# Kernel optimization log

Hardware: AMD Instinct MI355X
Metric: run time of the kernel (lower is better)

## Reference

```python
import math
import jax, jax.numpy as jnp
import numpy as np

EPS = 1e-4
FMAX = 18  # max filtersize for scale clamped to 2.5: ceil(3*2^2.5+0.5)=18 -> kernel 37x37
KSZ = 2 * FMAX + 1


def _conv2d(x, w, b):
    # 3x3 conv, padding 1, NCHW / OIHW (cross-correlation, matches torch)
    y = jax.lax.conv_general_dilated(x, w, (1, 1), [(1, 1), (1, 1)],
                                     dimension_numbers=('NCHW', 'OIHW', 'NCHW'))
    return y + b[None, :, None, None]


def _basis_filters(scale):
    # scale: [B] -> [B,3,K,K] (g, dgdx, dgdy), masked to the per-sample support
    std = 2.0 ** scale                              # [B]
    fs = jnp.ceil(3.0 * std + 0.5)                  # per-sample filtersize
    x = jnp.arange(-FMAX, FMAX + 1, dtype=jnp.float32)          # [K]
    m = (jnp.abs(x)[None, :] <= fs[:, None]).astype(jnp.float32)  # [B,K] support mask
    e = jnp.exp(-0.5 * (x[None, :] / std[:, None]) ** 2) * m      # masked 1D gaussian [B,K]
    g = e[:, :, None] * e[:, None, :]                              # [B,K,K]
    g = g / jnp.sum(g, axis=(1, 2), keepdims=True)
    c = (-x[None, :] / (std[:, None] ** 3 * 2.0 * math.pi)) * e    # [B,K]
    dgdx = c[:, :, None] * e[:, None, :]   # varies along first spatial dim (x[0])
    dgdx = dgdx / jnp.sum(jnp.abs(dgdx), axis=(1, 2), keepdims=True)
    dgdy = e[:, :, None] * c[:, None, :]   # varies along second spatial dim (x[1])
    dgdy = dgdy / jnp.sum(jnp.abs(dgdy), axis=(1, 2), keepdims=True)
    return jnp.stack([g, dgdx, dgdy], axis=1)  # [B,3,K,K]


def setup_inputs() -> dict:
    key = jax.random.key(0)
    ks = jax.random.split(key, 7)
    B, H, W = 8, 512, 512
    batch = jax.random.uniform(ks[0], (B, 3, H, W), dtype=jnp.float32)
    gcm = jnp.array([[0.06, 0.63, 0.27], [0.3, 0.04, -0.35], [0.34, -0.6, 0.17]],
                    dtype=jnp.float32)
    w1 = jax.random.normal(ks[1], (16, 3, 3, 3), dtype=jnp.float32) * 0.1
    b1 = jax.random.normal(ks[2], (16,), dtype=jnp.float32) * 0.01
    w2 = jax.random.normal(ks[3], (16, 16, 3, 3), dtype=jnp.float32) * 0.1
    b2 = jax.random.normal(ks[4], (16,), dtype=jnp.float32) * 0.01
    w3 = jax.random.normal(ks[5], (1, 16, 3, 3), dtype=jnp.float32) * 0.1
    b3 = jax.random.normal(ks[6], (1,), dtype=jnp.float32) * 0.01
    return {"batch": batch, "gcm": gcm, "w1": w1, "b1": b1,
            "w2": w2, "b2": b2, "w3": w3, "b3": b3}


def reference(batch, gcm, w1, b1, w2, b2, w3, b3):
    B, _, H, W = batch.shape
    # ---- RGB order prior (non-differentiable, no_grad in torch) ----
    oh = lambda i: jax.nn.one_hot(i, 3, axis=1, dtype=batch.dtype)
    mx = jnp.argmax(batch, axis=1)                 # first max
    mn = jnp.argmin(batch, axis=1)
    bf = batch[:, ::-1]
    mx2 = 2 - jnp.argmax(bf, axis=1)               # last max
    mn2 = 2 - jnp.argmin(bf, axis=1)
    RGB_order = jax.lax.stop_gradient(
        0.5 * (oh(mx) + oh(mx2)) - 0.5 * (oh(mn) + oh(mn2)))  # [B,3,H,W]

    # ---- per-sample adaptive scale from small CNN ----
    h = jax.nn.silu(_conv2d(batch, w1, b1))
    h = jax.nn.silu(_conv2d(h, w2, b2))
    s = _conv2d(h, w3, b3)
    scale = jnp.clip(jnp.mean(s, axis=(1, 2, 3)), -2.5, 2.5)   # [B]

    # ---- Gaussian color model ----
    xg = jnp.einsum('ij,bjhw->bihw', gcm, batch)  # [B,3,H,W] -> (E, El, Ell)

    # ---- per-sample Gaussian basis convolution, batched via grouped conv ----
    basis = _basis_filters(scale)                                  # [B,3,K,K]
    xin = xg.reshape(1, B * 3, H, W)
    wk = jnp.broadcast_to(basis[:, None], (B, 3, 3, KSZ, KSZ)).reshape(B * 9, 1, KSZ, KSZ)
    out = jax.lax.conv_general_dilated(xin, wk, (1, 1), [(FMAX, FMAX), (FMAX, FMAX)],
                                       feature_group_count=B * 3,
                                       dimension_numbers=('NCHW', 'OIHW', 'NCHW'))
    out = out.reshape(B, 3, 3, H, W)   # [B, chan(E/El/Ell), filt(g/dx/dy), H, W]
    E = out[:, 0, 0:1]
    Ex = out[:, 0, 1:2]
    Ey = out[:, 0, 2:3]
    El = out[:, 1, 0:1]
    Ell = out[:, 2, 0:1]

    Hf = jnp.arctan(El / (Ell + EPS))
    S = jnp.log((El ** 2 + Ell ** 2) / (E ** 2 + EPS) + EPS)
    Ww = jnp.arctan((Ex / (E + EPS)) ** 2 + (Ey / (E + EPS)) ** 2)
    return jnp.concatenate([Hf, S, RGB_order, Ww], axis=1)  # [B,6,H,W]
```

## Files before the change

kernel.cpp:

```cpp
#include <hip/hip_runtime.h>
#include <hip/hip_bf16.h>

constexpr int BN = 8, HH = 512, WW = 512;
constexpr int PIX = HH * WW;
constexpr float EPSF = 1e-4f;

__device__ __forceinline__ float b2f(__hip_bfloat16 x) { return __bfloat162float(x); }
__device__ __forceinline__ __hip_bfloat16 f2b(float x) { return __float2bfloat16(x); }
__device__ __forceinline__ unsigned short bfbits(float x) {
    union { __hip_bfloat16 b; unsigned short u; } cv; cv.b = f2b(x); return cv.u;
}
__device__ __forceinline__ unsigned int cvtpk(float lo, float hi) {
    unsigned int r;
    asm("v_cvt_pk_bf16_f32 %0, %1, %2" : "=v"(r) : "v"(lo), "v"(hi));
    return r;
}
__device__ __forceinline__ float silu(float a) {
    return a * __builtin_amdgcn_rcpf(1.f + __expf(-a));
}

typedef __attribute__((ext_vector_type(8))) short bf16x8;
typedef __attribute__((ext_vector_type(4))) float f32x4;

constexpr int OFF_TOT = 0;
constexpr int OFF_ROW0 = 128;
constexpr int OFF_ROW1 = 256;
constexpr int OFF_COL0 = 384;
constexpr int OFF_COL1 = 512;
constexpr int OFF_COR = 640;
constexpr int OFF_W1R = 1280;
constexpr int OFF_WR  = 2048;
constexpr int OFF_EH  = 4608;
constexpr int OFF_CH  = 5120;
constexpr size_t OFF_TPB = 65536;
constexpr size_t TP_BYTES = (size_t)4 * BN * PIX * 4;
constexpr size_t WS_NEEDED = OFF_TPB + TP_BYTES;

__global__ void prep_kernel(const float* __restrict__ w1, const float* __restrict__ w2,
                            float* __restrict__ wsf) {
    int t = threadIdx.x;
    for (int i = t; i < 640; i += 256) wsf[i] = 0.f;
    unsigned short* ab = (unsigned short*)(wsf + OFF_WR);
    for (int idx = t; idx < 5120; idx += 256) {
        int part = idx / 2560;
        int id = idx - part * 2560;
        int ks = id >> 9, rem = id & 511, lane = rem >> 3, j = id & 7;
        int oc = lane & 15, q = lane >> 4;
        int k = q * 8 + j;
        int tap = 2 * ks + (k >> 4), ic = k & 15;
        float val = (tap <= 8) ? w2[oc * 144 + ic * 9 + tap] : 0.f;
        float hv = b2f(f2b(val));
        ab[idx] = (part == 0) ? bfbits(val) : bfbits(val - hv);
    }
    unsigned short* a1 = (unsigned short*)(wsf + OFF_W1R);
    for (int idx = t; idx < 1024; idx += 256) {
        int part = idx >> 9;
        int id = idx & 511;
        int lane = id >> 3, j = id & 7;
        int oc = lane & 15, q = lane >> 4;
        int k = q * 8 + j;
        float val = (k < 27) ? w1[oc * 27 + k] : 0.f;
        float hv = b2f(f2b(val));
        a1[idx] = (part == 0) ? bfbits(val) : bfbits(val - hv);
    }
}

__global__ __launch_bounds__(256) void conv12_kernel(const float* __restrict__ batch,
                                                     const unsigned short* __restrict__ w1buf,
                                                     const float* __restrict__ b1,
                                                     const unsigned short* __restrict__ abuf,
                                                     const float* __restrict__ b2v,
                                                     float* __restrict__ wsf,
                                                     float* __restrict__ out) {
    __shared__ unsigned short stb[3][12][68];
    __shared__ uint4 h1s[10 * 66 * 2];
    __shared__ float part[4][16];

    int tx = threadIdx.x;
    int lane = tx & 63, wave = tx >> 6;
    int n = lane & 15, q = lane >> 4;
    int w0 = blockIdx.x * 64, h0 = blockIdx.y * 8, b = blockIdx.z;

    union { uint4 u; bf16x8 v; } cv;
    const float* pb = batch + (size_t)(b * 3) * PIX;

    unsigned int* stw = (unsigned int*)&stb[0][0][0];
    for (int i = tx; i < 1224; i += 256) {
        int ch = i / 408, rem = i - ch * 408;
        int r = rem / 34, c2 = rem - r * 34;
        int gh = h0 - 2 + r, gw = w0 - 2 + 2 * c2;
        const float* p = pb + (size_t)ch * PIX + (size_t)gh * WW;
        bool rok = (gh >= 0) && (gh < HH);
        float v0 = (rok && gw >= 0 && gw < WW) ? p[gw] : 0.f;
        float v1 = (rok && gw + 1 >= 0 && gw + 1 < WW) ? p[gw + 1] : 0.f;
        stw[i] = cvtpk(v0, v1);
    }

    bf16x8 w1h, w1l;
    const uint4* w14 = (const uint4*)w1buf;
    cv.u = w14[lane];      w1h = cv.v;
    cv.u = w14[64 + lane]; w1l = cv.v;
    int koff[8];
#pragma unroll
    for (int j = 0; j < 8; j++) {
        int k = q * 8 + j;
        int kk = (k < 27) ? k : 0;
        int ic = kk / 9, rem = kk - ic * 9, kh = rem / 3, kw = rem - kh * 3;
        koff[j] = ic * 816 + kh * 68 + kw;
    }
    float b1q[4];
#pragma unroll
    for (int r = 0; r < 4; r++) b1q[r] = b1[q * 4 + r];
    bool hiq = (q == 3);
    __syncthreads();

    const unsigned short* sptr = &stb[0][0][0];
    unsigned int* hw = (unsigned int*)h1s;
    int i_c = wave * 16 + n;
    int r_c = (unsigned)i_c / 66u; int c_c = i_c - r_c * 66;
    int base_c = r_c * 68 + c_c;
    unsigned short x0 = sptr[base_c + koff[0]], x1 = sptr[base_c + koff[1]];
    unsigned short x2 = sptr[base_c + koff[2]], x3 = sptr[base_c + koff[3]];
    unsigned short x4 = sptr[base_c + koff[4]], x5 = sptr[base_c + koff[5]];
    unsigned short x6 = sptr[base_c + koff[6]], x7 = sptr[base_c + koff[7]];
    int g = wave;
    for (int gi = 0; gi < 11; gi++) {
        unsigned short y0 = 0, y1 = 0, y2 = 0, y3 = 0, y4 = 0, y5 = 0, y6 = 0, y7 = 0;
        int i_n = 0, c_n = 0;
        if (gi < 10) {
            i_n = (g + 4) * 16 + n; if (i_n > 659) i_n = 659;
            int r_n = (unsigned)i_n / 66u; c_n = i_n - r_n * 66;
            int base_n = r_n * 68 + c_n;
            y0 = sptr[base_n + koff[0]]; y1 = sptr[base_n + koff[1]];
            y2 = sptr[base_n + koff[2]]; y3 = sptr[base_n + koff[3]];
            y4 = sptr[base_n + koff[4]]; y5 = sptr[base_n + koff[5]];
            y6 = sptr[base_n + koff[6]]; y7 = sptr[base_n + koff[7]];
        }
        union { unsigned int w[4]; bf16x8 v; } bb;
        bb.w[0] = (unsigned int)x0 | ((unsigned int)x1 << 16);
        bb.w[1] = (unsigned int)x2 | ((unsigned int)x3 << 16);
        bb.w[2] = (unsigned int)x4 | ((unsigned int)x5 << 16);
        bb.w[3] = (unsigned int)x6 | ((unsigned int)x7 << 16);
        if (hiq) {
            bb.w[1] &= 0xFFFFu; bb.w[2] = 0u; bb.w[3] = 0u;
        }
        f32x4 a = {0, 0, 0, 0};
        a = __builtin_amdgcn_mfma_f32_16x16x32_bf16(w1h, bb.v, a, 0, 0, 0);
        a = __builtin_amdgcn_mfma_f32_16x16x32_bf16(w1l, bb.v, a, 0, 0, 0);
        int rr_ = (unsigned)i_c / 66u;
        int gh = h0 - 1 + rr_, gw = w0 - 1 + c_c;
        bool ok = ((unsigned)gh < (unsigned)HH) && ((unsigned)gw < (unsigned)WW);
        unsigned int p0 = cvtpk(silu(a[0] + b1q[0]), silu(a[1] + b1q[1]));
        unsigned int p1 = cvtpk(silu(a[2] + b1q[2]), silu(a[3] + b1q[3]));
        p0 = ok ? p0 : 0u;
        p1 = ok ? p1 : 0u;
        int swz = (c_c >> 2) & 1;
        int slot = i_c * 2 + ((q >= 2) ? (swz ^ 1) : swz);
        *(uint2*)&hw[slot * 4 + (q & 1) * 2] = make_uint2(p0, p1);
        x0 = y0; x1 = y1; x2 = y2; x3 = y3; x4 = y4; x5 = y5; x6 = y6; x7 = y7;
        i_c = i_n; c_c = c_n;
        g += 4;
    }

    for (int j = tx; j < 512; j += 256) {
        int rr = j >> 6, ccx = j & 63;
        size_t p = (size_t)(h0 + rr) * WW + (w0 + ccx);
        float v0 = pb[p], v1 = pb[(size_t)PIX + p], v2 = pb[2 * (size_t)PIX + p];
        int mx  = (v0 >= v1 && v0 >= v2) ? 0 : ((v1 >= v2) ? 1 : 2);
        int mx2 = (v2 >= v1 && v2 >= v0) ? 2 : ((v1 >= v0) ? 1 : 0);
        int mn  = (v0 <= v1 && v0 <= v2) ? 0 : ((v1 <= v2) ? 1 : 2);
        int mn2 = (v2 <= v1 && v2 <= v0) ? 2 : ((v1 <= v0) ? 1 : 0);
#pragma unroll
        for (int c = 0; c < 3; c++) {
            float r = 0.5f * ((float)(c == mx) + (float)(c == mx2))
                    - 0.5f * ((float)(c == mn) + (float)(c == mn2));
            out[(size_t)(b * 6 + 2 + c) * PIX + p] = r;
        }
    }
    __syncthreads();

    bf16x8 ah[5], al[5];
    const uint4* ab4 = (const uint4*)abuf;
#pragma unroll
    for (int ks = 0; ks < 5; ks++) {
        cv.u = ab4[ks * 64 + lane];       ah[ks] = cv.v;
        cv.u = ab4[320 + ks * 64 + lane]; al[ks] = cv.v;
    }
    float b2q[4];
#pragma unroll
    for (int r = 0; r < 4; r++) b2q[r] = b2v[q * 4 + r];

    float tt[4] = {0, 0, 0, 0};
    float cs0[4] = {0, 0, 0, 0};
    float cs1[4] = {0, 0, 0, 0};
    for (int rloc = 0; rloc < 2; rloc++) {
        int row = wave * 2 + rloc;
        int grow = h0 + row;
        f32x4 acc[4] = {{0,0,0,0},{0,0,0,0},{0,0,0,0},{0,0,0,0}};
#pragma unroll
        for (int ks = 0; ks < 5; ks++) {
            int tap = 2 * ks + (q >> 1); if (tap > 8) tap = 8;
            int dh = tap / 3 - 1, dw = tap % 3 - 1;
            int half = q & 1;
            int lr = row + 1 + dh;
#pragma unroll
            for (int t = 0; t < 4; t++) {
                int c = 1 + dw + t * 16 + n;
                cv.u = h1s[(lr * 66 + c) * 2 + (half ^ ((c >> 2) & 1))];
                acc[t] = __builtin_amdgcn_mfma_f32_16x16x32_bf16(ah[ks], cv.v, acc[t], 0, 0, 0);
                acc[t] = __builtin_amdgcn_mfma_f32_16x16x32_bf16(al[ks], cv.v, acc[t], 0, 0, 0);
            }
        }
        float sv[4][4];
#pragma unroll
        for (int t = 0; t < 4; t++)
#pragma unroll
            for (int r = 0; r < 4; r++)
                sv[t][r] = silu(acc[t][r] + b2q[r]);
#pragma unroll
        for (int r = 0; r < 4; r++) tt[r] += sv[0][r] + sv[1][r] + sv[2][r] + sv[3][r];
        if (grow == 0 || grow == HH - 1) {
            int off = (grow == 0) ? OFF_ROW0 : OFF_ROW1;
#pragma unroll
            for (int r = 0; r < 4; r++) {
                float x = sv[0][r] + sv[1][r] + sv[2][r] + sv[3][r];
#pragma unroll
                for (int d = 1; d < 16; d <<= 1) x += __shfl_xor(x, d, 64);
                if (n == 0) atomicAdd(&wsf[off + b * 16 + q * 4 + r], x);
            }
        }
        if (blockIdx.x == 0 && n == 0)
#pragma unroll
            for (int r = 0; r < 4; r++) cs0[r] += sv[0][r];
        if (blockIdx.x == 7 && n == 15)
#pragma unroll
            for (int r = 0; r < 4; r++) cs1[r] += sv[3][r];
        if ((grow == 0 || grow == HH - 1)) {
            int hi = (grow == 0) ? 0 : 1;
            if (blockIdx.x == 0 && n == 0)
#pragma unroll
                for (int r = 0; r < 4; r++)
                    wsf[OFF_COR + ((b * 2 + hi) * 2 + 0) * 16 + q * 4 + r] = sv[0][r];
            if (blockIdx.x == 7 && n == 15)
#pragma unroll
                for (int r = 0; r < 4; r++)
                    wsf[OFF_COR + ((b * 2 + hi) * 2 + 1) * 16 + q * 4 + r] = sv[3][r];
        }
    }
    if (blockIdx.x == 0 && n == 0)
#pragma unroll
        for (int r = 0; r < 4; r++) atomicAdd(&wsf[OFF_COL0 + b * 16 + q * 4 + r], cs0[r]);
    if (blockIdx.x == 7 && n == 15)
#pragma unroll
        for (int r = 0; r < 4; r++) atomicAdd(&wsf[OFF_COL1 + b * 16 + q * 4 + r], cs1[r]);
#pragma unroll
    for (int r = 0; r < 4; r++) {
        float x = tt[r];
#pragma unroll
        for (int d = 1; d < 16; d <<= 1) x += __shfl_xor(x, d, 64);
        tt[r] = x;
    }
    if (n == 0)
#pragma unroll
        for (int r = 0; r < 4; r++) part[wave][q * 4 + r] = tt[r];
    __syncthreads();
    if (tx < 16)
        atomicAdd(&wsf[OFF_TOT + b * 16 + tx],
                  part[0][tx] + part[1][tx] + part[2][tx] + part[3][tx]);
}

__global__ void filter_kernel(const float* __restrict__ w3, const float* __restrict__ b3,
                              float* __restrict__ wsf) {
    int b = blockIdx.x, t = threadIdx.x;
    __shared__ float red[160];
    float val = 0.f;
    if (t < 144) {
        int ic = t / 9, tap = t % 9, kh = tap / 3, kw = tap % 3;
        float T = wsf[OFF_TOT + b * 16 + ic];
        int hi = -1, wi = -1;
        if (kh == 0) { T -= wsf[OFF_ROW1 + b * 16 + ic]; hi = 1; }
        else if (kh == 2) { T -= wsf[OFF_ROW0 + b * 16 + ic]; hi = 0; }
        if (kw == 0) { T -= wsf[OFF_COL1 + b * 16 + ic]; wi = 1; }
        else if (kw == 2) { T -= wsf[OFF_COL0 + b * 16 + ic]; wi = 0; }
        if (hi >= 0 && wi >= 0) T += wsf[OFF_COR + ((b * 2 + hi) * 2 + wi) * 16 + ic];
        val = w3[t] * T;
    }
    red[t] = val;
    __syncthreads();
    __shared__ float sh_mean;
    if (t == 0) {
        float S = 0.f;
        for (int i = 0; i < 144; i++) S += red[i];
        sh_mean = b3[0] + S * (1.f / (float)PIX);
    }
    __syncthreads();
    float scale = fminf(2.5f, fmaxf(-2.5f, sh_mean));
    float sd = exp2f(scale);
    float fs = ceilf(3.f * sd + 0.5f);
    float e = 0.f, c = 0.f;
    if (t < 37) {
        float x = (float)(t - 18);
        if (fabsf(x) <= fs) {
            float qq = x / sd;
            e = __expf(-0.5f * qq * qq);
            c = -x / (sd * sd * sd * 6.28318530717958647692f) * e;
        }
    }
    __shared__ float sa[40], sb[40];
    if (t < 37) { sa[t] = e; sb[t] = fabsf(c); }
    __syncthreads();
    __shared__ float Se, Sc;
    if (t == 0) {
        float a = 0.f, d = 0.f;
        for (int i = 0; i < 37; i++) { a += sa[i]; d += sb[i]; }
        Se = a; Sc = d;
    }
    __syncthreads();
    if (t < 37) {
        wsf[OFF_EH + b * 37 + t] = e / Se;
        wsf[OFF_CH + b * 37 + t] = c / Sc;
    }
}

__device__ __forceinline__ int skw(int c) { return c + (c >> 5); }
__global__ __launch_bounds__(256, 4) void horiz_kernel(const float* __restrict__ batch,
                                                       const float* __restrict__ gcm,
                                                       const float* __restrict__ ehat,
                                                       const float* __restrict__ chat,
                                                       float* __restrict__ t) {
    __shared__ float xr[2][3][566];
    __shared__ float cE[40], cC[40];
    int tx = threadIdx.x;
    int h0 = blockIdx.x * 2;
    int b  = blockIdx.y;
    if (tx < 37) { cE[tx] = ehat[b * 37 + tx]; cC[tx] = chat[b * 37 + tx]; }
    const float* pb = batch + (size_t)(b * 3) * PIX;
    float g0 = gcm[0], g1 = gcm[1], g2 = gcm[2];
    float g3 = gcm[3], g4 = gcm[4], g5 = gcm[5];
    float g6 = gcm[6], g7 = gcm[7], g8 = gcm[8];
    for (int i = tx; i < 2 * 548; i += 256) {
        int r = i / 548, c = i - r * 548;
        int gw = c - 18;
        float v0 = 0.f, v1 = 0.f, v2 = 0.f;
        if (gw >= 0 && gw < WW) {
            size_t p = (size_t)(h0 + r) * WW + gw;
            v0 = pb[p]; v1 = pb[(size_t)PIX + p]; v2 = pb[2 * (size_t)PIX + p];
        }
        int cs = skw(c);
        xr[r][0][cs] = g0 * v0 + g1 * v1 + g2 * v2;
        xr[r][1][cs] = g3 * v0 + g4 * v1 + g5 * v2;
        xr[r][2][cs] = g6 * v0 + g7 * v1 + g8 * v2;
    }
    __syncthreads();
    int r = tx >> 7, colbase = (tx & 127) * 4;
    float a0[4] = {}, a1[4] = {}, a2[4] = {}, a3[4] = {};
    float e1, e2, e3, d1, d2, d3;
    {
        float ce[3], cc2[3];
#pragma unroll
        for (int k = 0; k < 3; k++) { ce[k] = cE[k]; cc2[k] = cC[k]; }
#pragma unroll
        for (int kk = 0; kk < 3; kk++) {
            int cs = skw(colbase + kk);
            float x0 = xr[r][0][cs], x1 = xr[r][1][cs], x2 = xr[r][2][cs];
#pragma unroll
            for (int i = 0; i < 3; i++) {
                if (i <= kk) {
                    float ce_ = ce[kk - i], cc_ = cc2[kk - i];
                    a0[i] += ce_ * x0; a1[i] += ce_ * x1;
                    a2[i] += ce_ * x2; a3[i] += cc_ * x0;
                }
            }
        }
        e1 = ce[2]; e2 = ce[1]; e3 = ce[0];
        d1 = cc2[2]; d2 = cc2[1]; d3 = cc2[0];
    }
#pragma unroll 2
    for (int kk = 3; kk < 37; kk++) {
        float e0 = cE[kk], d0 = cC[kk];
        int cs = skw(colbase + kk);
        float x0 = xr[r][0][cs], x1 = xr[r][1][cs], x2 = xr[r][2][cs];
        a0[0] += e0 * x0; a1[0] += e0 * x1; a2[0] += e0 * x2; a3[0] += d0 * x0;
        a0[1] += e1 * x0; a1[1] += e1 * x1; a2[1] += e1 * x2; a3[1] += d1 * x0;
        a0[2] += e2 * x0; a1[2] += e2 * x1; a2[2] += e2 * x2; a3[2] += d2 * x0;
        a0[3] += e3 * x0; a1[3] += e3 * x1; a2[3] += e3 * x2; a3[3] += d3 * x0;
        e3 = e2; e2 = e1; e1 = e0; d3 = d2; d2 = d1; d1 = d0;
    }
    {
        int cs = skw(colbase + 37);
        float x0 = xr[r][0][cs], x1 = xr[r][1][cs], x2 = xr[r][2][cs];
        a0[1] += e1 * x0; a1[1] += e1 * x1; a2[1] += e1 * x2; a3[1] += d1 * x0;
        a0[2] += e2 * x0; a1[2] += e2 * x1; a2[2] += e2 * x2; a3[2] += d2 * x0;
        a0[3] += e3 * x0; a1[3] += e3 * x1; a2[3] += e3 * x2; a3[3] += d3 * x0;
    }
    {
        int cs = skw(colbase + 38);
        float x0 = xr[r][0][cs], x1 = xr[r][1][cs], x2 = xr[r][2][cs];
        a0[2] += e1 * x0; a1[2] += e1 * x1; a2[2] += e1 * x2; a3[2] += d1 * x0;
        a0[3] += e2 * x0; a1[3] += e2 * x1; a2[3] += e2 * x2; a3[3] += d2 * x0;
    }
    {
        int cs = skw(colbase + 39);
        float x0 = xr[r][0][cs], x1 = xr[r][1][cs], x2 = xr[r][2][cs];
        a0[3] += e1 * x0; a1[3] += e1 * x1; a2[3] += e1 * x2; a3[3] += d1 * x0;
    }
    const size_t PL = (size_t)BN * PIX;
    size_t p = (size_t)b * PIX + (size_t)(h0 + r) * WW + colbase;
    *(float4*)&t[0 * PL + p] = make_float4(a0[0], a0[1], a0[2], a0[3]);
    *(float4*)&t[1 * PL + p] = make_float4(a1[0], a1[1], a1[2], a1[3]);
    *(float4*)&t[2 * PL + p] = make_float4(a2[0], a2[1], a2[2], a2[3]);
    *(float4*)&t[3 * PL + p] = make_float4(a3[0], a3[1], a3[2], a3[3]);
}

#define VACC(ee, dd, ii) { E[ii] += (ee) * v0; Ex[ii] += (dd) * v0; Ey[ii] += (ee) * v3; \
                           El[ii] += (ee) * v1; Ell[ii] += (ee) * v2; }
__global__ __launch_bounds__(256, 4) void vert_kernel(const float* __restrict__ t,
                                                      const float* __restrict__ ehat,
                                                      const float* __restrict__ chat,
                                                      float* __restrict__ out) {
    __shared__ float cE[40], cC[40];
    int tx = threadIdx.x;
    int b = blockIdx.z;
    if (tx < 37) { cE[tx] = ehat[b * 37 + tx]; cC[tx] = chat[b * 37 + tx]; }
    int j = blockIdx.x * 64 + (tx & 63);
    int r0 = (blockIdx.y * 4 + (tx >> 6)) * 4;
    const size_t PL = (size_t)BN * PIX;
    const float* t0 = t + (size_t)b * PIX;
    __syncthreads();
    float E[4] = {}, Ex[4] = {}, Ey[4] = {}, El[4] = {}, Ell[4] = {};
    bool safe = (r0 >= 18) && (r0 <= HH - 22);
    float e1, e2, e3, d1, d2, d3;
    {
        float ce[3], cc2[3];
#pragma unroll
        for (int k = 0; k < 3; k++) { ce[k] = cE[k]; cc2[k] = cC[k]; }
#pragma unroll
        for (int kk = 0; kk < 3; kk++) {
            int gr = r0 - 18 + kk;
            float v0 = 0.f, v1 = 0.f, v2 = 0.f, v3 = 0.f;
            if ((unsigned)gr < (unsigned)HH) {
                size_t idx = (size_t)gr * WW + j;
                v0 = t0[idx]; v1 = t0[PL + idx]; v2 = t0[2 * PL + idx]; v3 = t0[3 * PL + idx];
            }
#pragma unroll
            for (int i = 0; i < 3; i++) {
                if (i <= kk) {
                    float ee = ce[kk - i], dd = cc2[kk - i];
                    VACC(ee, dd, i)
                }
            }
        }
        e1 = ce[2]; e2 = ce[1]; e3 = ce[0];
        d1 = cc2[2]; d2 = cc2[1]; d3 = cc2[0];
    }
    const float* pv = t0 + (size_t)(r0 - 15) * WW + j;
    if (safe) {
#pragma unroll 2
        for (int kk = 3; kk < 37; kk++) {
            float e0 = cE[kk], d0 = cC[kk];
            float v0 = pv[0], v1 = pv[PL], v2 = pv[2 * PL], v3 = pv[3 * PL];
            VACC(e0, d0, 0) VACC(e1, d1, 1) VACC(e2, d2, 2) VACC(e3, d3, 3)
            e3 = e2; e2 = e1; e1 = e0; d3 = d2; d2 = d1; d1 = d0;
            pv += WW;
        }
    } else {
        int gr = r0 - 15;
#pragma unroll 2
        for (int kk = 3; kk < 37; kk++) {
            float e0 = cE[kk], d0 = cC[kk];
            float v0 = 0.f, v1 = 0.f, v2 = 0.f, v3 = 0.f;
            if ((unsigned)gr < (unsigned)HH) {
                v0 = pv[0]; v1 = pv[PL]; v2 = pv[2 * PL]; v3 = pv[3 * PL];
            }
            VACC(e0, d0, 0) VACC(e1, d1, 1) VACC(e2, d2, 2) VACC(e3, d3, 3)
            e3 = e2; e2 = e1; e1 = e0; d3 = d2; d2 = d1; d1 = d0;
            pv += WW; gr++;
        }
    }
#pragma unroll
    for (int kk = 37; kk < 40; kk++) {
        int gr = r0 - 18 + kk;
        float v0 = 0.f, v1 = 0.f, v2 = 0.f, v3 = 0.f;
        if (gr < HH) {
            size_t idx = (size_t)gr * WW + j;
            v0 = t0[idx]; v1 = t0[PL + idx]; v2 = t0[2 * PL + idx]; v3 = t0[3 * PL + idx];
        }
        if (kk == 37) { VACC(e1, d1, 1) VACC(e2, d2, 2) VACC(e3, d3, 3) }
        if (kk == 38) { VACC(e1, d1, 2) VACC(e2, d2, 3) }
        if (kk == 39) { VACC(e1, d1, 3) }
    }
#pragma unroll
    for (int i = 0; i < 4; i++) {
        int h = r0 + i;
        float Hf = atanf(El[i] / (Ell[i] + EPSF));
        float S = logf((El[i] * El[i] + Ell[i] * Ell[i]) / (E[i] * E[i] + EPSF) + EPSF);
        float rx = Ex[i] / (E[i] + EPSF), ry = Ey[i] / (E[i] + EPSF);
        float Wv = atanf(rx * rx + ry * ry);
        size_t base = (size_t)(b * 6) * PIX + (size_t)h * WW + j;
        out[base] = Hf;
        out[base + PIX] = S;
        out[base + 5 * (size_t)PIX] = Wv;
    }
}
#undef VACC

extern "C" void kernel_launch(void* const* d_in, const int* in_sizes, int n_in,
                              void* d_out, int out_size, void* d_ws, size_t ws_size,
                              hipStream_t stream) {
    const float* batch = (const float*)d_in[0];
    const float* gcm   = (const float*)d_in[1];
    const float* w1    = (const float*)d_in[2];
    const float* b1    = (const float*)d_in[3];
    const float* w2    = (const float*)d_in[4];
    const float* b2    = (const float*)d_in[5];
    const float* w3    = (const float*)d_in[6];
    const float* b3    = (const float*)d_in[7];
    float* out = (float*)d_out;

    if (ws_size < WS_NEEDED) return;

    float* wsf = (float*)d_ws;
    float* tpl = (float*)((char*)d_ws + OFF_TPB);
    float* ehat = wsf + OFF_EH;
    float* chat = wsf + OFF_CH;

    prep_kernel<<<dim3(1), dim3(256), 0, stream>>>(w1, w2, wsf);
    conv12_kernel<<<dim3(8, 64, 8), dim3(256), 0, stream>>>(
        batch, (const unsigned short*)(wsf + OFF_W1R), b1,
        (const unsigned short*)(wsf + OFF_WR), b2, wsf, out);
    filter_kernel<<<dim3(8), dim3(160), 0, stream>>>(w3, b3, wsf);
    horiz_kernel<<<dim3(256, 8), dim3(256), 0, stream>>>(batch, gcm, ehat, chat, tpl);
    vert_kernel<<<dim3(8, 32, 8), dim3(256), 0, stream>>>(tpl, ehat, chat, out);
}
```

Before: 233.0 us.

## Run separable Gaussian convolutions as banded bf16 MFMA matmuls with split precision

The horizontal and vertical 37-tap passes move from scalar FMA loops onto MFMA. The filter kernel now builds banded Toeplitz A-fragments of the 1D Gaussian and its derivative, split into bf16 hi/mid/lo parts. Inputs are split into bf16 components so the products approach fp32 accuracy. The intermediate is stored transposed, with bf16 for the E and Ey planes and fp32 for El/Ell. This replaces many FMAs with fewer matrix instructions and cuts intermediate traffic, at the cost of lower precision on some planes and extra splitting work.

```diff
diff --git a/kernel.cpp b/kernel.cpp
--- a/kernel.cpp
+++ b/kernel.cpp
@@ -10,6 +10,9 @@
 __device__ __forceinline__ unsigned short bfbits(float x) {
     union { __hip_bfloat16 b; unsigned short u; } cv; cv.b = f2b(x); return cv.u;
 }
+__device__ __forceinline__ float ubf(unsigned short u) {
+    union { unsigned int i; float f; } c; c.i = ((unsigned int)u) << 16; return c.f;
+}
 __device__ __forceinline__ unsigned int cvtpk(float lo, float hi) {
     unsigned int r;
     asm("v_cvt_pk_bf16_f32 %0, %1, %2" : "=v"(r) : "v"(lo), "v"(hi));
@@ -21,6 +24,16 @@
 
 typedef __attribute__((ext_vector_type(8))) short bf16x8;
 typedef __attribute__((ext_vector_type(4))) float f32x4;
+
+#define MF(acc, A, B) (acc) = __builtin_amdgcn_mfma_f32_16x16x32_bf16((A), (B), (acc), 0, 0, 0)
+
+__device__ __forceinline__ bf16x8 ldb(const unsigned short* s, int off16) {
+    const uint2* p = (const uint2*)(s + off16);
+    uint2 a = p[0], c = p[1];
+    union { uint4 u; bf16x8 v; } cv;
+    cv.u = make_uint4(a.x, a.y, c.x, c.y);
+    return cv.v;
+}
 
 constexpr int OFF_TOT = 0;
 constexpr int OFF_ROW0 = 128;
@@ -30,11 +43,14 @@
 constexpr int OFF_COR = 640;
 constexpr int OFF_W1R = 1280;
 constexpr int OFF_WR  = 2048;
-constexpr int OFF_EH  = 4608;
-constexpr int OFF_CH  = 5120;
-constexpr size_t OFF_TPB = 65536;
-constexpr size_t TP_BYTES = (size_t)4 * BN * PIX * 4;
-constexpr size_t WS_NEEDED = OFF_TPB + TP_BYTES;
+constexpr int OFF_AFR = 8192;
+constexpr size_t OFF_TP0 = 262144;
+constexpr size_t SZ_TPH = (size_t)BN * PIX * 2;
+constexpr size_t SZ_TPF = (size_t)BN * PIX * 4;
+constexpr size_t OFF_TP1 = OFF_TP0 + SZ_TPH;
+constexpr size_t OFF_TP2 = OFF_TP1 + SZ_TPF;
+constexpr size_t OFF_TP3 = OFF_TP2 + SZ_TPF;
+constexpr size_t WS_NEEDED = OFF_TP3 + SZ_TPH;
 
 __global__ void prep_kernel(const float* __restrict__ w1, const float* __restrict__ w2,
                             float* __restrict__ wsf) {
@@ -145,8 +161,8 @@
             bb.w[1] &= 0xFFFFu; bb.w[2] = 0u; bb.w[3] = 0u;
         }
         f32x4 a = {0, 0, 0, 0};
-        a = __builtin_amdgcn_mfma_f32_16x16x32_bf16(w1h, bb.v, a, 0, 0, 0);
-        a = __builtin_amdgcn_mfma_f32_16x16x32_bf16(w1l, bb.v, a, 0, 0, 0);
+        MF(a, w1h, bb.v);
+        MF(a, w1l, bb.v);
         int rr_ = (unsigned)i_c / 66u;
         int gh = h0 - 1 + rr_, gw = w0 - 1 + c_c;
         bool ok = ((unsigned)gh < (unsigned)HH) && ((unsigned)gw < (unsigned)WW);
@@ -207,8 +223,8 @@
             for (int t = 0; t < 4; t++) {
                 int c = 1 + dw + t * 16 + n;
                 cv.u = h1s[(lr * 66 + c) * 2 + (half ^ ((c >> 2) & 1))];
-                acc[t] = __builtin_amdgcn_mfma_f32_16x16x32_bf16(ah[ks], cv.v, acc[t], 0, 0, 0);
-                acc[t] = __builtin_amdgcn_mfma_f32_16x16x32_bf16(al[ks], cv.v, acc[t], 0, 0, 0);
+                MF(acc[t], ah[ks], cv.v);
+                MF(acc[t], al[ks], cv.v);
             }
         }
         float sv[4][4];
@@ -306,203 +322,197 @@
             c = -x / (sd * sd * sd * 6.28318530717958647692f) * e;
         }
     }
-    __shared__ float sa[40], sb[40];
-    if (t < 37) { sa[t] = e; sb[t] = fabsf(c); }
+    __shared__ float sa[40], sb2[40];
+    if (t < 37) { sa[t] = e; sb2[t] = fabsf(c); }
     __syncthreads();
     __shared__ float Se, Sc;
     if (t == 0) {
         float a = 0.f, d = 0.f;
-        for (int i = 0; i < 37; i++) { a += sa[i]; d += sb[i]; }
+        for (int i = 0; i < 37; i++) { a += sa[i]; d += sb2[i]; }
         Se = a; Sc = d;
     }
     __syncthreads();
-    if (t < 37) {
-        wsf[OFF_EH + b * 37 + t] = e / Se;
-        wsf[OFF_CH + b * 37 + t] = c / Sc;
-    }
-}
-
-__device__ __forceinline__ int skw(int c) { return c + (c >> 5); }
-__global__ __launch_bounds__(256, 4) void horiz_kernel(const float* __restrict__ batch,
-                                                       const float* __restrict__ gcm,
-                                                       const float* __restrict__ ehat,
-                                                       const float* __restrict__ chat,
-                                                       float* __restrict__ t) {
-    __shared__ float xr[2][3][566];
-    __shared__ float cE[40], cC[40];
+    __shared__ float sEn[37], sCn[37];
+    if (t < 37) { sEn[t] = e / Se; sCn[t] = c / Sc; }
+    __syncthreads();
+    if (t < 64) {
+        int r = t & 15, q = t >> 4;
+        uint4* afr = (uint4*)(wsf + OFF_AFR) + (size_t)b * 640 + t;
+#pragma unroll
+        for (int ks = 0; ks < 2; ks++) {
+            unsigned short eh[8], em[8], el[8], chp[8], cmp[8];
+#pragma unroll
+            for (int j2 = 0; j2 < 8; j2++) {
+                int d = ks * 32 + q * 8 + j2 - r;
+                bool ok = (d >= 0) && (d <= 36);
+                float ve = ok ? sEn[ok ? d : 0] : 0.f;
+                float vc = ok ? sCn[ok ? d : 0] : 0.f;
+                eh[j2] = bfbits(ve);
+                float r1 = ve - ubf(eh[j2]);
+                em[j2] = bfbits(r1);
+                el[j2] = bfbits(r1 - ubf(em[j2]));
+                chp[j2] = bfbits(vc);
+                cmp[j2] = bfbits(vc - ubf(chp[j2]));
+            }
+#define PK2(a0, a1) ((unsigned)(a0) | ((unsigned)(a1) << 16))
+            afr[(ks * 3 + 0) * 64] = make_uint4(PK2(eh[0], eh[1]), PK2(eh[2], eh[3]), PK2(eh[4], eh[5]), PK2(eh[6], eh[7]));
+            afr[(ks * 3 + 1) * 64] = make_uint4(PK2(em[0], em[1]), PK2(em[2], em[3]), PK2(em[4], em[5]), PK2(em[6], em[7]));
+            afr[(ks * 3 + 2) * 64] = make_uint4(PK2(el[0], el[1]), PK2(el[2], el[3]), PK2(el[4], el[5]), PK2(el[6], el[7]));
+            afr[(6 + ks * 2 + 0) * 64] = make_uint4(PK2(chp[0], chp[1]), PK2(chp[2], chp[3]), PK2(chp[4], chp[5]), PK2(chp[6], chp[7]));
+            afr[(6 + ks * 2 + 1) * 64] = make_uint4(PK2(cmp[0], cmp[1]), PK2(cmp[2], cmp[3]), PK2(cmp[4], cmp[5]), PK2(cmp[6], cmp[7]));
+#undef PK2
+        }
+    }
+}
+
+__global__ __launch_bounds__(256) void horiz_kernel(const float* __restrict__ batch,
+                                                    const float* __restrict__ gcm,
+                                                    const float* __restrict__ wsf,
+                                                    unsigned short* __restrict__ tp0,
+                                                    float* __restrict__ tp1,
+                                                    float* __restrict__ tp2,
+                                                    unsigned short* __restrict__ tp3) {
+    __shared__ unsigned short sx[7 * 32 * 84];
     int tx = threadIdx.x;
-    int h0 = blockIdx.x * 2;
-    int b  = blockIdx.y;
-    if (tx < 37) { cE[tx] = ehat[b * 37 + tx]; cC[tx] = chat[b * 37 + tx]; }
+    int lane = tx & 63, wave = tx >> 6;
+    int n = lane & 15, q = lane >> 4;
+    int j0 = blockIdx.x * 32, h0 = blockIdx.y * 32, b = blockIdx.z;
     const float* pb = batch + (size_t)(b * 3) * PIX;
     float g0 = gcm[0], g1 = gcm[1], g2 = gcm[2];
     float g3 = gcm[3], g4 = gcm[4], g5 = gcm[5];
     float g6 = gcm[6], g7 = gcm[7], g8 = gcm[8];
-    for (int i = tx; i < 2 * 548; i += 256) {
-        int r = i / 548, c = i - r * 548;
-        int gw = c - 18;
+    for (int i = tx; i < 2560; i += 256) {
+        int hh = i / 80, sc = i - hh * 80;
+        int gc = j0 - 18 + sc;
         float v0 = 0.f, v1 = 0.f, v2 = 0.f;
-        if (gw >= 0 && gw < WW) {
-            size_t p = (size_t)(h0 + r) * WW + gw;
+        if ((unsigned)gc < (unsigned)WW) {
+            size_t p = (size_t)(h0 + hh) * WW + gc;
             v0 = pb[p]; v1 = pb[(size_t)PIX + p]; v2 = pb[2 * (size_t)PIX + p];
         }
-        int cs = skw(c);
-        xr[r][0][cs] = g0 * v0 + g1 * v1 + g2 * v2;
-        xr[r][1][cs] = g3 * v0 + g4 * v1 + g5 * v2;
-        xr[r][2][cs] = g6 * v0 + g7 * v1 + g8 * v2;
-    }
-    __syncthreads();
-    int r = tx >> 7, colbase = (tx & 127) * 4;
-    float a0[4] = {}, a1[4] = {}, a2[4] = {}, a3[4] = {};
-    float e1, e2, e3, d1, d2, d3;
-    {
-        float ce[3], cc2[3];
-#pragma unroll
-        for (int k = 0; k < 3; k++) { ce[k] = cE[k]; cc2[k] = cC[k]; }
-#pragma unroll
-        for (int kk = 0; kk < 3; kk++) {
-            int cs = skw(colbase + kk);
-            float x0 = xr[r][0][cs], x1 = xr[r][1][cs], x2 = xr[r][2][cs];
-#pragma unroll
-            for (int i = 0; i < 3; i++) {
-                if (i <= kk) {
-                    float ce_ = ce[kk - i], cc_ = cc2[kk - i];
-                    a0[i] += ce_ * x0; a1[i] += ce_ * x1;
-                    a2[i] += ce_ * x2; a3[i] += cc_ * x0;
-                }
-            }
-        }
-        e1 = ce[2]; e2 = ce[1]; e3 = ce[0];
-        d1 = cc2[2]; d2 = cc2[1]; d3 = cc2[0];
-    }
-#pragma unroll 2
-    for (int kk = 3; kk < 37; kk++) {
-        float e0 = cE[kk], d0 = cC[kk];
-        int cs = skw(colbase + kk);
-        float x0 = xr[r][0][cs], x1 = xr[r][1][cs], x2 = xr[r][2][cs];
-        a0[0] += e0 * x0; a1[0] += e0 * x1; a2[0] += e0 * x2; a3[0] += d0 * x0;
-        a0[1] += e1 * x0; a1[1] += e1 * x1; a2[1] += e1 * x2; a3[1] += d1 * x0;
-        a0[2] += e2 * x0; a1[2] += e2 * x1; a2[2] += e2 * x2; a3[2] += d2 * x0;
-        a0[3] += e3 * x0; a1[3] += e3 * x1; a2[3] += e3 * x2; a3[3] += d3 * x0;
-        e3 = e2; e2 = e1; e1 = e0; d3 = d2; d2 = d1; d1 = d0;
-    }
-    {
-        int cs = skw(colbase + 37);
-        float x0 = xr[r][0][cs], x1 = xr[r][1][cs], x2 = xr[r][2][cs];
-        a0[1] += e1 * x0; a1[1] += e1 * x1; a2[1] += e1 * x2; a3[1] += d1 * x0;
-        a0[2] += e2 * x0; a1[2] += e2 * x1; a2[2] += e2 * x2; a3[2] += d2 * x0;
-        a0[3] += e3 * x0; a1[3] += e3 * x1; a2[3] += e3 * x2; a3[3] += d3 * x0;
-    }
-    {
-        int cs = skw(colbase + 38);
-        float x0 = xr[r][0][cs], x1 = xr[r][1][cs], x2 = xr[r][2][cs];
-        a0[2] += e1 * x0; a1[2] += e1 * x1; a2[2] += e1 * x2; a3[2] += d1 * x0;
-        a0[3] += e2 * x0; a1[3] += e2 * x1; a2[3] += e2 * x2; a3[3] += d2 * x0;
-    }
-    {
-        int cs = skw(colbase + 39);
-        float x0 = xr[r][0][cs], x1 = xr[r][1][cs], x2 = xr[r][2][cs];
-        a0[3] += e1 * x0; a1[3] += e1 * x1; a2[3] += e1 * x2; a3[3] += d1 * x0;
-    }
-    const size_t PL = (size_t)BN * PIX;
-    size_t p = (size_t)b * PIX + (size_t)(h0 + r) * WW + colbase;
-    *(float4*)&t[0 * PL + p] = make_float4(a0[0], a0[1], a0[2], a0[3]);
-    *(float4*)&t[1 * PL + p] = make_float4(a1[0], a1[1], a1[2], a1[3]);
-    *(float4*)&t[2 * PL + p] = make_float4(a2[0], a2[1], a2[2], a2[3]);
-    *(float4*)&t[3 * PL + p] = make_float4(a3[0], a3[1], a3[2], a3[3]);
-}
-
-#define VACC(ee, dd, ii) { E[ii] += (ee) * v0; Ex[ii] += (dd) * v0; Ey[ii] += (ee) * v3; \
-                           El[ii] += (ee) * v1; Ell[ii] += (ee) * v2; }
-__global__ __launch_bounds__(256, 4) void vert_kernel(const float* __restrict__ t,
-                                                      const float* __restrict__ ehat,
-                                                      const float* __restrict__ chat,
-                                                      float* __restrict__ out) {
-    __shared__ float cE[40], cC[40];
+        float x0 = g0 * v0 + g1 * v1 + g2 * v2;
+        float x1 = g3 * v0 + g4 * v1 + g5 * v2;
+        float x2 = g6 * v0 + g7 * v1 + g8 * v2;
+        int o = hh * 84 + sc;
+        sx[o] = bfbits(x0);
+        unsigned short h1 = bfbits(x1); sx[2688 + o] = h1;
+        float r1 = x1 - ubf(h1); unsigned short m1 = bfbits(r1); sx[2 * 2688 + o] = m1;
+        sx[3 * 2688 + o] = bfbits(r1 - ubf(m1));
+        unsigned short h2 = bfbits(x2); sx[4 * 2688 + o] = h2;
+        float r2 = x2 - ubf(h2); unsigned short m2 = bfbits(r2); sx[5 * 2688 + o] = m2;
+        sx[6 * 2688 + o] = bfbits(r2 - ubf(m2));
+    }
+    const uint4* afr = (const uint4*)(wsf + OFF_AFR) + (size_t)b * 640 + lane;
+    union { uint4 u; bf16x8 v; } cv;
+    bf16x8 Ae[2][3], Ac[2][2];
+#pragma unroll
+    for (int ks = 0; ks < 2; ks++) {
+#pragma unroll
+        for (int p = 0; p < 3; p++) { cv.u = afr[(ks * 3 + p) * 64]; Ae[ks][p] = cv.v; }
+#pragma unroll
+        for (int p = 0; p < 2; p++) { cv.u = afr[(6 + ks * 2 + p) * 64]; Ac[ks][p] = cv.v; }
+    }
+    __syncthreads();
+    int jt = wave & 1, ht = wave >> 1;
+    f32x4 a0 = {0,0,0,0}, a1 = {0,0,0,0}, a2 = {0,0,0,0}, a3 = {0,0,0,0};
+    int rb = (ht * 16 + n) * 84 + jt * 16 + q * 8;
+#pragma unroll
+    for (int ks = 0; ks < 2; ks++) {
+        int rk = rb + ks * 32;
+        bf16x8 B0  = ldb(sx, rk);
+        bf16x8 B1h = ldb(sx, 2688 + rk), B1m = ldb(sx, 2 * 2688 + rk), B1l = ldb(sx, 3 * 2688 + rk);
+        bf16x8 B2h = ldb(sx, 4 * 2688 + rk), B2m = ldb(sx, 5 * 2688 + rk), B2l = ldb(sx, 6 * 2688 + rk);
+        MF(a0, Ae[ks][0], B0); MF(a0, Ae[ks][1], B0);
+        MF(a3, Ac[ks][0], B0); MF(a3, Ac[ks][1], B0);
+        MF(a1, Ae[ks][0], B1h); MF(a1, Ae[ks][0], B1m); MF(a1, Ae[ks][1], B1h);
+        MF(a1, Ae[ks][0], B1l); MF(a1, Ae[ks][2], B1h); MF(a1, Ae[ks][1], B1m);
+        MF(a2, Ae[ks][0], B2h); MF(a2, Ae[ks][0], B2m); MF(a2, Ae[ks][1], B2h);
+        MF(a2, Ae[ks][0], B2l); MF(a2, Ae[ks][2], B2h); MF(a2, Ae[ks][1], B2m);
+    }
+    int jo = j0 + jt * 16 + q * 4;
+    int ho = h0 + ht * 16 + n;
+#pragma unroll
+    for (int r = 0; r < 4; r++) {
+        size_t ix = ((size_t)b * 512 + (jo + r)) * 512 + ho;
+        tp0[ix] = bfbits(a0[r]);
+        tp1[ix] = a1[r];
+        tp2[ix] = a2[r];
+        tp3[ix] = bfbits(a3[r]);
+    }
+}
+
+__global__ __launch_bounds__(256) void vert_kernel(const float* __restrict__ wsf,
+                                                   const unsigned short* __restrict__ tp0,
+                                                   const float* __restrict__ tp1,
+                                                   const float* __restrict__ tp2,
+                                                   const unsigned short* __restrict__ tp3,
+                                                   float* __restrict__ out) {
+    __shared__ unsigned short sb[8 * 32 * 84];
     int tx = threadIdx.x;
-    int b = blockIdx.z;
-    if (tx < 37) { cE[tx] = ehat[b * 37 + tx]; cC[tx] = chat[b * 37 + tx]; }
-    int j = blockIdx.x * 64 + (tx & 63);
-    int r0 = (blockIdx.y * 4 + (tx >> 6)) * 4;
-    const size_t PL = (size_t)BN * PIX;
-    const float* t0 = t + (size_t)b * PIX;
-    __syncthreads();
-    float E[4] = {}, Ex[4] = {}, Ey[4] = {}, El[4] = {}, Ell[4] = {};
-    bool safe = (r0 >= 18) && (r0 <= HH - 22);
-    float e1, e2, e3, d1, d2, d3;
-    {
-        float ce[3], cc2[3];
-#pragma unroll
-        for (int k = 0; k < 3; k++) { ce[k] = cE[k]; cc2[k] = cC[k]; }
-#pragma unroll
-        for (int kk = 0; kk < 3; kk++) {
-            int gr = r0 - 18 + kk;
-            float v0 = 0.f, v1 = 0.f, v2 = 0.f, v3 = 0.f;
-            if ((unsigned)gr < (unsigned)HH) {
-                size_t idx = (size_t)gr * WW + j;
-                v0 = t0[idx]; v1 = t0[PL + idx]; v2 = t0[2 * PL + idx]; v3 = t0[3 * PL + idx];
-            }
-#pragma unroll
-            for (int i = 0; i < 3; i++) {
-                if (i <= kk) {
-                    float ee = ce[kk - i], dd = cc2[kk - i];
-                    VACC(ee, dd, i)
-                }
-            }
-        }
-        e1 = ce[2]; e2 = ce[1]; e3 = ce[0];
-        d1 = cc2[2]; d2 = cc2[1]; d3 = cc2[0];
-    }
-    const float* pv = t0 + (size_t)(r0 - 15) * WW + j;
-    if (safe) {
-#pragma unroll 2
-        for (int kk = 3; kk < 37; kk++) {
-            float e0 = cE[kk], d0 = cC[kk];
-            float v0 = pv[0], v1 = pv[PL], v2 = pv[2 * PL], v3 = pv[3 * PL];
-            VACC(e0, d0, 0) VACC(e1, d1, 1) VACC(e2, d2, 2) VACC(e3, d3, 3)
-            e3 = e2; e2 = e1; e1 = e0; d3 = d2; d2 = d1; d1 = d0;
-            pv += WW;
-        }
-    } else {
-        int gr = r0 - 15;
-#pragma unroll 2
-        for (int kk = 3; kk < 37; kk++) {
-            float e0 = cE[kk], d0 = cC[kk];
-            float v0 = 0.f, v1 = 0.f, v2 = 0.f, v3 = 0.f;
-            if ((unsigned)gr < (unsigned)HH) {
-                v0 = pv[0]; v1 = pv[PL]; v2 = pv[2 * PL]; v3 = pv[3 * PL];
-            }
-            VACC(e0, d0, 0) VACC(e1, d1, 1) VACC(e2, d2, 2) VACC(e3, d3, 3)
-            e3 = e2; e2 = e1; e1 = e0; d3 = d2; d2 = d1; d1 = d0;
-            pv += WW; gr++;
-        }
-    }
-#pragma unroll
-    for (int kk = 37; kk < 40; kk++) {
-        int gr = r0 - 18 + kk;
-        float v0 = 0.f, v1 = 0.f, v2 = 0.f, v3 = 0.f;
-        if (gr < HH) {
-            size_t idx = (size_t)gr * WW + j;
-            v0 = t0[idx]; v1 = t0[PL + idx]; v2 = t0[2 * PL + idx]; v3 = t0[3 * PL + idx];
-        }
-        if (kk == 37) { VACC(e1, d1, 1) VACC(e2, d2, 2) VACC(e3, d3, 3) }
-        if (kk == 38) { VACC(e1, d1, 2) VACC(e2, d2, 3) }
-        if (kk == 39) { VACC(e1, d1, 3) }
-    }
-#pragma unroll
-    for (int i = 0; i < 4; i++) {
-        int h = r0 + i;
-        float Hf = atanf(El[i] / (Ell[i] + EPSF));
-        float S = logf((El[i] * El[i] + Ell[i] * Ell[i]) / (E[i] * E[i] + EPSF) + EPSF);
-        float rx = Ex[i] / (E[i] + EPSF), ry = Ey[i] / (E[i] + EPSF);
+    int lane = tx & 63, wave = tx >> 6;
+    int n = lane & 15, q = lane >> 4;
+    int j0 = blockIdx.x * 32, r0 = blockIdx.y * 32, b = blockIdx.z;
+    for (int i = tx; i < 2560; i += 256) {
+        int jj = i / 80, sr = i - jj * 80;
+        int gh = r0 - 18 + sr;
+        unsigned short w0 = 0, w7 = 0; float f1 = 0.f, f2 = 0.f;
+        if ((unsigned)gh < (unsigned)HH) {
+            size_t ix = ((size_t)b * 512 + (j0 + jj)) * 512 + gh;
+            w0 = tp0[ix]; f1 = tp1[ix]; f2 = tp2[ix]; w7 = tp3[ix];
+        }
+        int o = jj * 84 + sr;
+        sb[o] = w0;
+        unsigned short h1 = bfbits(f1); sb[2688 + o] = h1;
+        float r1 = f1 - ubf(h1); unsigned short m1 = bfbits(r1); sb[2 * 2688 + o] = m1;
+        sb[3 * 2688 + o] = bfbits(r1 - ubf(m1));
+        unsigned short h2 = bfbits(f2); sb[4 * 2688 + o] = h2;
+        float r2 = f2 - ubf(h2); unsigned short m2 = bfbits(r2); sb[5 * 2688 + o] = m2;
+        sb[6 * 2688 + o] = bfbits(r2 - ubf(m2));
+        sb[7 * 2688 + o] = w7;
+    }
+    const uint4* afr = (const uint4*)(wsf + OFF_AFR) + (size_t)b * 640 + lane;
+    union { uint4 u; bf16x8 v; } cv;
+    bf16x8 Ae[2][3], Ac[2][2];
+#pragma unroll
+    for (int ks = 0; ks < 2; ks++) {
+#pragma unroll
+        for (int p = 0; p < 3; p++) { cv.u = afr[(ks * 3 + p) * 64]; Ae[ks][p] = cv.v; }
+#pragma unroll
+        for (int p = 0; p < 2; p++) { cv.u = afr[(6 + ks * 2 + p) * 64]; Ac[ks][p] = cv.v; }
+    }
+    __syncthreads();
+    int ct = wave & 1, rt = wave >> 1;
+    f32x4 aE = {0,0,0,0}, aX = {0,0,0,0}, aY = {0,0,0,0}, aL = {0,0,0,0}, aLL = {0,0,0,0};
+    int rb = (ct * 16 + n) * 84 + rt * 16 + q * 8;
+#pragma unroll
+    for (int ks = 0; ks < 2; ks++) {
+        int rk = rb + ks * 32;
+        bf16x8 B0  = ldb(sb, rk);
+        bf16x8 B1h = ldb(sb, 2688 + rk), B1m = ldb(sb, 2 * 2688 + rk), B1l = ldb(sb, 3 * 2688 + rk);
+        bf16x8 B2h = ldb(sb, 4 * 2688 + rk), B2m = ldb(sb, 5 * 2688 + rk), B2l = ldb(sb, 6 * 2688 + rk);
+        bf16x8 B3  = ldb(sb, 7 * 2688 + rk);
+        MF(aE, Ae[ks][0], B0); MF(aE, Ae[ks][1], B0);
+        MF(aX, Ac[ks][0], B0); MF(aX, Ac[ks][1], B0);
+        MF(aY, Ae[ks][0], B3); MF(aY, Ae[ks][1], B3);
+        MF(aL, Ae[ks][0], B1h); MF(aL, Ae[ks][0], B1m); MF(aL, Ae[ks][1], B1h);
+        MF(aL, Ae[ks][0], B1l); MF(aL, Ae[ks][2], B1h); MF(aL, Ae[ks][1], B1m);
+        MF(aLL, Ae[ks][0], B2h); MF(aLL, Ae[ks][0], B2m); MF(aLL, Ae[ks][1], B2h);
+        MF(aLL, Ae[ks][0], B2l); MF(aLL, Ae[ks][2], B2h); MF(aLL, Ae[ks][1], B2m);
+    }
+    int ho = r0 + rt * 16 + q * 4;
+    int jo = j0 + ct * 16 + n;
+#pragma unroll
+    for (int r = 0; r < 4; r++) {
+        float E = aE[r], Ex = aX[r], Ey = aY[r], El = aL[r], Ell = aLL[r];
+        float Hf = atanf(El / (Ell + EPSF));
+        float S = logf((El * El + Ell * Ell) / (E * E + EPSF) + EPSF);
+        float rx = Ex / (E + EPSF), ry = Ey / (E + EPSF);
         float Wv = atanf(rx * rx + ry * ry);
-        size_t base = (size_t)(b * 6) * PIX + (size_t)h * WW + j;
+        size_t base = (size_t)(b * 6) * PIX + (size_t)(ho + r) * WW + jo;
         out[base] = Hf;
         out[base + PIX] = S;
         out[base + 5 * (size_t)PIX] = Wv;
     }
 }
-#undef VACC
 
 extern "C" void kernel_launch(void* const* d_in, const int* in_sizes, int n_in,
                               void* d_out, int out_size, void* d_ws, size_t ws_size,
@@ -520,15 +530,16 @@
     if (ws_size < WS_NEEDED) return;
 
     float* wsf = (float*)d_ws;
-    float* tpl = (float*)((char*)d_ws + OFF_TPB);
-    float* ehat = wsf + OFF_EH;
-    float* chat = wsf + OFF_CH;
+    unsigned short* tp0 = (unsigned short*)((char*)d_ws + OFF_TP0);
+    float* tp1 = (float*)((char*)d_ws + OFF_TP1);
+    float* tp2 = (float*)((char*)d_ws + OFF_TP2);
+    unsigned short* tp3 = (unsigned short*)((char*)d_ws + OFF_TP3);
 
     prep_kernel<<<dim3(1), dim3(256), 0, stream>>>(w1, w2, wsf);
     conv12_kernel<<<dim3(8, 64, 8), dim3(256), 0, stream>>>(
         batch, (const unsigned short*)(wsf + OFF_W1R), b1,
         (const unsigned short*)(wsf + OFF_WR), b2, wsf, out);
     filter_kernel<<<dim3(8), dim3(160), 0, stream>>>(w3, b3, wsf);
-    horiz_kernel<<<dim3(256, 8), dim3(256), 0, stream>>>(batch, gcm, ehat, chat, tpl);
-    vert_kernel<<<dim3(8, 32, 8), dim3(256), 0, stream>>>(tpl, ehat, chat, out);
-}
+    horiz_kernel<<<dim3(16, 16, 8), dim3(256), 0, stream>>>(batch, gcm, wsf, tp0, tp1, tp2, tp3);
+    vert_kernel<<<dim3(16, 16, 8), dim3(256), 0, stream>>>(wsf, tp0, tp1, tp2, tp3, out);
+}
```

Measured after the change: 229.5 us. No clear change (-1.5%).
